# Performance work log

Hardware: AMD Instinct MI355X
Metric: run time of the kernel (lower is better)

## Reference

```python
import jax, jax.numpy as jnp
import numpy as np

K_LAYERS = 10
ALPHA = 0.1
N_NODES = 100_000
N_EDGES = 1_600_000
D_FEAT = 64


def setup_inputs() -> dict:
    key = jax.random.key(0)
    k1, k2, k3 = jax.random.split(key, 3)
    features = jax.random.normal(k1, (N_NODES, D_FEAT), dtype=jnp.float32)
    src = jax.random.randint(k2, (N_EDGES,), 0, N_NODES, dtype=jnp.int64)
    dst = jax.random.randint(k3, (N_EDGES,), 0, N_NODES, dtype=jnp.int64)
    return {"features": features, "src": src, "dst": dst}


def reference(features, src, dst):
    # APPNP forward (eval mode: feature dropout and edge_drop are identity).
    n = features.shape[0]
    ones = jnp.ones((src.shape[0],), dtype=features.dtype)
    deg_out = jax.ops.segment_sum(ones, src, num_segments=n)
    deg_in = jax.ops.segment_sum(ones, dst, num_segments=n)
    norm_src = jnp.clip(deg_out, 1.0) ** -0.5  # [N]
    norm_dst = jnp.clip(deg_in, 1.0) ** -0.5   # [N]

    h0 = features
    h = features
    for _ in range(K_LAYERS):
        # D_out^{-1/2} scaling, gather to edges, scatter-sum to dst, D_in^{-1/2}
        msg = (h * norm_src[:, None])[src]               # [E, d]
        agg = jax.ops.segment_sum(msg, dst, num_segments=n)  # [N, d]
        h = (1.0 - ALPHA) * (agg * norm_dst[:, None]) + ALPHA * h0
    return h
```

## Files before the change

kernel.cpp:

```cpp
#include <hip/hip_runtime.h>
#include <hip/hip_fp16.h>
#include <stdint.h>

#define D_FEAT 64
#define K_LAYERS 10
#define SCAN_CHUNK 2048
#define BINS 32768

__global__ __launch_bounds__(256) void deg_rank_hist_kernel(
    const int* __restrict__ src, const int* __restrict__ dst,
    int* deg_in, int* __restrict__ rank,
    unsigned short* __restrict__ Hsrc, int E, int N, int histBlocks)
{
    __shared__ unsigned ls[BINS / 4];
    int b = blockIdx.x;
    if (b >= histBlocks) {
        int i = (b - histBlocks) * blockDim.x + threadIdx.x;
        int base = i * 4;
        if (base + 3 < E) {
            int4 d4 = *(const int4*)(dst + base);
            int4 r;
            r.x = atomicAdd(&deg_in[d4.x], 1);
            r.y = atomicAdd(&deg_in[d4.y], 1);
            r.z = atomicAdd(&deg_in[d4.z], 1);
            r.w = atomicAdd(&deg_in[d4.w], 1);
            *(int4*)(rank + base) = r;
        } else {
            for (int j = base; j < E; ++j)
                rank[j] = atomicAdd(&deg_in[dst[j]], 1);
        }
    } else {
        int stripe = (((E + histBlocks - 1) / histBlocks) + 3) & ~3;
        int begin = b * stripe;
        int endb  = min(E, begin + stripe);
        int npass = (N + BINS - 1) / BINS;
        for (int p = 0; p < npass; ++p) {
            for (int j = threadIdx.x; j < BINS / 4; j += 256) ls[j] = 0;
            __syncthreads();
            unsigned lo = (unsigned)p * BINS;
            for (int q = begin + (int)threadIdx.x * 4; q < endb; q += 256 * 4) {
                if (q + 3 < endb) {
                    int4 s4 = *(const int4*)(src + q);
                    unsigned k;
                    k = (unsigned)s4.x - lo; if (k < BINS) atomicAdd(&ls[k >> 2], 1u << (8 * (k & 3)));
                    k = (unsigned)s4.y - lo; if (k < BINS) atomicAdd(&ls[k >> 2], 1u << (8 * (k & 3)));
                    k = (unsigned)s4.z - lo; if (k < BINS) atomicAdd(&ls[k >> 2], 1u << (8 * (k & 3)));
                    k = (unsigned)s4.w - lo; if (k < BINS) atomicAdd(&ls[k >> 2], 1u << (8 * (k & 3)));
                } else {
                    for (int t = q; t < endb; ++t) {
                        unsigned k = (unsigned)src[t] - lo;
                        if (k < BINS) atomicAdd(&ls[k >> 2], 1u << (8 * (k & 3)));
                    }
                }
            }
            __syncthreads();
            int nv = min(BINS, N - (int)lo);
            unsigned* HS = (unsigned*)(Hsrc + (size_t)b * N + lo);
            for (int j = threadIdx.x; j < nv / 4; j += 256) {
                unsigned w = ls[j];
                HS[2 * j]     = (w & 0xffu) | ((w >> 8) & 0xffu) << 16;
                HS[2 * j + 1] = ((w >> 16) & 0xffu) | ((w >> 24) & 0xffu) << 16;
            }
            __syncthreads();
        }
    }
}

__global__ void norm_kernel(const unsigned short* __restrict__ Hsrc,
                            const int* __restrict__ deg_in,
                            float* __restrict__ ns, float* __restrict__ nd,
                            float* __restrict__ cvec, int N, int histBlocks)
{
    int t = blockIdx.x * blockDim.x + threadIdx.x;
    int v0 = t * 4;
    if (v0 >= N) return;
    unsigned so[4] = {0, 0, 0, 0};
#pragma unroll 8
    for (int b = 0; b < histBlocks; ++b) {
        ushort4 h = *(const ushort4*)(Hsrc + (size_t)b * N + v0);
        so[0] += h.x; so[1] += h.y; so[2] += h.z; so[3] += h.w;
    }
    int4 di = *(const int4*)(deg_in + v0);
    float4 a, bb, cv;
    a.x = rsqrtf(fmaxf((float)so[0], 1.0f));
    a.y = rsqrtf(fmaxf((float)so[1], 1.0f));
    a.z = rsqrtf(fmaxf((float)so[2], 1.0f));
    a.w = rsqrtf(fmaxf((float)so[3], 1.0f));
    bb.x = rsqrtf(fmaxf((float)di.x, 1.0f));
    bb.y = rsqrtf(fmaxf((float)di.y, 1.0f));
    bb.z = rsqrtf(fmaxf((float)di.z, 1.0f));
    bb.w = rsqrtf(fmaxf((float)di.w, 1.0f));
    cv.x = 0.9f * a.x * bb.x;
    cv.y = 0.9f * a.y * bb.y;
    cv.z = 0.9f * a.z * bb.z;
    cv.w = 0.9f * a.w * bb.w;
    *(float4*)(ns + v0)   = a;
    *(float4*)(nd + v0)   = bb;
    *(float4*)(cvec + v0) = cv;
}

__global__ void chunk_sum_kernel(const int* __restrict__ deg, int N, int* __restrict__ partials) {
    __shared__ int sdata[256];
    constexpr int PT = SCAN_CHUNK / 256;
    int base = blockIdx.x * SCAN_CHUNK;
    int t = threadIdx.x;
    int s = 0;
#pragma unroll
    for (int j = 0; j < PT; ++j) {
        int idx = base + t * PT + j;
        if (idx < N) s += deg[idx];
    }
    sdata[t] = s;
    __syncthreads();
    for (int off = 128; off > 0; off >>= 1) {
        if (t < off) sdata[t] += sdata[t + off];
        __syncthreads();
    }
    if (t == 0) partials[blockIdx.x] = sdata[0];
}

__global__ void scan_partials_kernel(int* partials, int nchunks, int* row_ptr, int N, int E) {
    if (threadIdx.x == 0 && blockIdx.x == 0) {
        int s = 0;
        for (int i = 0; i < nchunks; ++i) { int v = partials[i]; partials[i] = s; s += v; }
        row_ptr[N] = E;
    }
}

__global__ void chunk_scan_kernel(const int* __restrict__ deg, int N,
                                  const int* __restrict__ partials, int* __restrict__ row_ptr) {
    __shared__ int sdata[256];
    constexpr int PT = SCAN_CHUNK / 256;
    int base = blockIdx.x * SCAN_CHUNK;
    int t = threadIdx.x;
    int vals[PT];
    int s = 0;
#pragma unroll
    for (int j = 0; j < PT; ++j) {
        int idx = base + t * PT + j;
        int v = (idx < N) ? deg[idx] : 0;
        vals[j] = s;
        s += v;
    }
    sdata[t] = s;
    __syncthreads();
    for (int off = 1; off < 256; off <<= 1) {
        int v = (t >= off) ? sdata[t - off] : 0;
        __syncthreads();
        sdata[t] += v;
        __syncthreads();
    }
    int texcl = (t > 0) ? sdata[t - 1] : 0;
    int off0 = partials[blockIdx.x];
#pragma unroll
    for (int j = 0; j < PT; ++j) {
        int idx = base + t * PT + j;
        if (idx < N) row_ptr[idx] = off0 + texcl + vals[j];
    }
}

__global__ void fill_cvt_kernel(const int* __restrict__ src, const int* __restrict__ dst,
                                const int* __restrict__ rank, const int* __restrict__ row_ptr,
                                unsigned* __restrict__ edge_src, int E, int fillBlocks,
                                const float* __restrict__ features, const float* __restrict__ ns,
                                __half* __restrict__ g0, __half* __restrict__ f0g, int N) {
    int b = blockIdx.x;
    if (b < fillBlocks) {
        int i = b * blockDim.x + threadIdx.x;
        int base = i * 4;
        if (base + 3 < E) {
            int4 s4 = *(const int4*)(src + base);
            int4 d4 = *(const int4*)(dst + base);
            int4 r4 = *(const int4*)(rank + base);
            edge_src[row_ptr[d4.x] + r4.x] = (unsigned)s4.x;
            edge_src[row_ptr[d4.y] + r4.y] = (unsigned)s4.y;
            edge_src[row_ptr[d4.z] + r4.z] = (unsigned)s4.z;
            edge_src[row_ptr[d4.w] + r4.w] = (unsigned)s4.w;
        } else {
            for (int j = base; j < E; ++j)
                edge_src[row_ptr[dst[j]] + rank[j]] = (unsigned)src[j];
        }
    } else {
        int t = (b - fillBlocks) * blockDim.x + threadIdx.x;
        if (t < N * (D_FEAT / 8)) {
            int node = t >> 3;
            float s = ns[node];
            float4 a = *((const float4*)features + 2 * t);
            float4 c = *((const float4*)features + 2 * t + 1);
            __half2 og[4], of[4];
            og[0] = __float22half2_rn(make_float2(s * a.x, s * a.y));
            og[1] = __float22half2_rn(make_float2(s * a.z, s * a.w));
            og[2] = __float22half2_rn(make_float2(s * c.x, s * c.y));
            og[3] = __float22half2_rn(make_float2(s * c.z, s * c.w));
            float sf = 0.1f * s;
            of[0] = __float22half2_rn(make_float2(sf * a.x, sf * a.y));
            of[1] = __float22half2_rn(make_float2(sf * a.z, sf * a.w));
            of[2] = __float22half2_rn(make_float2(sf * c.x, sf * c.y));
            of[3] = __float22half2_rn(make_float2(sf * c.z, sf * c.w));
            *((float4*)g0 + t)  = *(const float4*)og;
            *((float4*)f0g + t) = *(const float4*)of;
        }
    }
}

template <bool LAST>
__global__ __launch_bounds__(256) void prop_kernel(
    const __half* __restrict__ g, const __half* __restrict__ f0g,
    const float* __restrict__ features,
    const unsigned* __restrict__ edge_src, const int* __restrict__ row_ptr,
    const float* __restrict__ cvec, const float* __restrict__ nd,
    void* __restrict__ out, int N)
{
    int tid  = blockIdx.x * blockDim.x + threadIdx.x;
    int wave = tid >> 6;
    int lane = threadIdx.x & 63;
    int grp  = lane >> 3;
    int fl   = lane & 7;
    int node = wave * 8 + grp;
    if (node >= N) return;

    int e   = row_ptr[node];
    int end = row_ptr[node + 1];

    float acc[8];
#pragma unroll
    for (int j = 0; j < 8; ++j) acc[j] = 0.f;

    for (; e + 2 <= end; e += 2) {
        unsigned s0 = edge_src[e];
        unsigned s1 = edge_src[e + 1];
        float4 v0 = *((const float4*)(g + ((size_t)s0 << 6)) + fl);
        float4 v1 = *((const float4*)(g + ((size_t)s1 << 6)) + fl);
        const __half2* p0 = (const __half2*)&v0;
        const __half2* p1 = (const __half2*)&v1;
#pragma unroll
        for (int k = 0; k < 4; ++k) {
            float2 f0 = __half22float2(p0[k]);
            float2 f1 = __half22float2(p1[k]);
            acc[2 * k]     += f0.x + f1.x;
            acc[2 * k + 1] += f0.y + f1.y;
        }
    }
    if (e < end) {
        unsigned s0 = edge_src[e];
        float4 v0 = *((const float4*)(g + ((size_t)s0 << 6)) + fl);
        const __half2* p0 = (const __half2*)&v0;
#pragma unroll
        for (int k = 0; k < 4; ++k) {
            float2 f0 = __half22float2(p0[k]);
            acc[2 * k]     += f0.x;
            acc[2 * k + 1] += f0.y;
        }
    }

    if (!LAST) {
        float cm = cvec[node];
        float4 braw = *((const float4*)(f0g + ((size_t)node << 6)) + fl);
        const __half2* bp = (const __half2*)&braw;
        __half2 o[4];
#pragma unroll
        for (int k = 0; k < 4; ++k) {
            float2 f = __half22float2(bp[k]);
            o[k] = __float22half2_rn(make_float2(fmaf(cm, acc[2 * k], f.x),
                                                 fmaf(cm, acc[2 * k + 1], f.y)));
        }
        *((float4*)((__half*)out + ((size_t)node << 6)) + fl) = *(const float4*)o;
    } else {
        float w = 0.9f * nd[node];
        const float4* fp = (const float4*)(features + ((size_t)node << 6));
        float4 b0 = fp[2 * fl];
        float4 b1 = fp[2 * fl + 1];
        float4 o0, o1;
        o0.x = fmaf(w, acc[0], 0.1f * b0.x);
        o0.y = fmaf(w, acc[1], 0.1f * b0.y);
        o0.z = fmaf(w, acc[2], 0.1f * b0.z);
        o0.w = fmaf(w, acc[3], 0.1f * b0.w);
        o1.x = fmaf(w, acc[4], 0.1f * b1.x);
        o1.y = fmaf(w, acc[5], 0.1f * b1.y);
        o1.z = fmaf(w, acc[6], 0.1f * b1.z);
        o1.w = fmaf(w, acc[7], 0.1f * b1.w);
        float4* op = (float4*)((float*)out + ((size_t)node << 6));
        op[2 * fl]     = o0;
        op[2 * fl + 1] = o1;
    }
}

extern "C" void kernel_launch(void* const* d_in, const int* in_sizes, int n_in,
                              void* d_out, int out_size, void* d_ws, size_t ws_size,
                              hipStream_t stream) {
    const float* features = (const float*)d_in[0];
    const int*   src      = (const int*)d_in[1];
    const int*   dst      = (const int*)d_in[2];
    const int E = in_sizes[1];
    const int N = in_sizes[0] / D_FEAT;

    char* ws = (char*)d_ws;
    size_t off = 0;
    auto alloc = [&](size_t bytes, size_t align) -> char* {
        off = (off + align - 1) & ~(align - 1);
        char* p = ws + off;
        off += bytes;
        return p;
    };
    int*            deg_in    = (int*)alloc(4 * (size_t)N, 4);
    int*            row_ptr   = (int*)alloc(4 * ((size_t)N + 1), 4);
    float*          ns        = (float*)alloc(4 * (size_t)N, 4);
    float*          nd        = (float*)alloc(4 * (size_t)N, 4);
    float*          cvec      = (float*)alloc(4 * (size_t)N, 4);
    int nchunks = (N + SCAN_CHUNK - 1) / SCAN_CHUNK;
    int*            spartials = (int*)alloc(4 * (size_t)nchunks, 4);
    int*            rank      = (int*)alloc(4 * (size_t)E, 16);
    unsigned*       edge_src  = (unsigned*)alloc(4 * (size_t)E, 16);
    __half*         f0g       = (__half*)alloc(2 * (size_t)N * D_FEAT, 16);
    __half*         gA        = (__half*)alloc(2 * (size_t)N * D_FEAT, 16);
    __half*         gB        = (__half*)alloc(2 * (size_t)N * D_FEAT, 16);
    size_t remain = (ws_size > off + 1024) ? (ws_size - off - 1024) : 0;
    int HBr = (int)(remain / (2 * (size_t)N));
    HBr = HBr > 256 ? 256 : HBr;
    HBr = (HBr / 64) * 64;
    if (HBr < 64) HBr = 64;
    unsigned short* Hsrc = (unsigned short*)alloc(2 * (size_t)HBr * N, 16);

    (void)hipMemsetAsync(deg_in, 0, 4 * (size_t)N, stream);

    int ethreads4 = (E + 3) / 4;
    int eblocks = (ethreads4 + 255) / 256;
    deg_rank_hist_kernel<<<HBr + eblocks, 256, 0, stream>>>(src, dst, deg_in, rank, Hsrc, E, N, HBr);
    norm_kernel<<<(N / 4 + 255) / 256, 256, 0, stream>>>(Hsrc, deg_in, ns, nd, cvec, N, HBr);
    chunk_sum_kernel<<<nchunks, 256, 0, stream>>>(deg_in, N, spartials);
    scan_partials_kernel<<<1, 64, 0, stream>>>(spartials, nchunks, row_ptr, N, E);
    chunk_scan_kernel<<<nchunks, 256, 0, stream>>>(deg_in, N, spartials, row_ptr);

    int cvtThreads = N * (D_FEAT / 8);
    int cvtBlocks = (cvtThreads + 255) / 256;
    fill_cvt_kernel<<<eblocks + cvtBlocks, 256, 0, stream>>>(
        src, dst, rank, row_ptr, edge_src, E, eblocks, features, ns, gA, f0g, N);

    int waves = (N + 7) / 8;
    int prop_blocks = (waves * 64 + 255) / 256;
    const __half* h_in = gA;
    for (int k = 0; k < K_LAYERS - 1; ++k) {
        __half* h_out = (k & 1) ? gA : gB;
        prop_kernel<false><<<prop_blocks, 256, 0, stream>>>(
            h_in, f0g, features, edge_src, row_ptr, cvec, nd, h_out, N);
        h_in = h_out;
    }
    prop_kernel<true><<<prop_blocks, 256, 0, stream>>>(
        h_in, f0g, features, edge_src, row_ptr, cvec, nd, d_out, N);
}
```

Before: 672.6 us.

## Fuse all propagation layers into one persistent cooperative kernel with grid sync

Replaces the ten separate propagation launches with a single cooperative persistent kernel. It loops over layers, uses grid-stride node assignment and calls grid.sync between layers, ping-ponging the two half-precision buffers. This removes per-layer launch overhead and tail effects. In exchange it adds grid-wide barrier cost, and the grid is sized from occupancy (capped at 2048 blocks, assuming 256 CUs), so it may run with fewer waves in flight than the original launch.

```diff
diff --git a/kernel.cpp b/kernel.cpp
--- a/kernel.cpp
+++ b/kernel.cpp
@@ -1,6 +1,9 @@
 #include <hip/hip_runtime.h>
 #include <hip/hip_fp16.h>
+#include <hip/hip_cooperative_groups.h>
 #include <stdint.h>
+
+namespace cg = cooperative_groups;
 
 #define D_FEAT 64
 #define K_LAYERS 10
@@ -203,85 +206,95 @@
     }
 }
 
-template <bool LAST>
-__global__ __launch_bounds__(256) void prop_kernel(
-    const __half* __restrict__ g, const __half* __restrict__ f0g,
-    const float* __restrict__ features,
+__global__ __launch_bounds__(256, 8) void prop_persist_kernel(
+    __half* __restrict__ gA, __half* __restrict__ gB,
+    const __half* __restrict__ f0g, const float* __restrict__ features,
     const unsigned* __restrict__ edge_src, const int* __restrict__ row_ptr,
     const float* __restrict__ cvec, const float* __restrict__ nd,
-    void* __restrict__ out, int N)
+    float* __restrict__ out, int N)
 {
-    int tid  = blockIdx.x * blockDim.x + threadIdx.x;
-    int wave = tid >> 6;
-    int lane = threadIdx.x & 63;
-    int grp  = lane >> 3;
-    int fl   = lane & 7;
-    int node = wave * 8 + grp;
-    if (node >= N) return;
-
-    int e   = row_ptr[node];
-    int end = row_ptr[node + 1];
-
-    float acc[8];
-#pragma unroll
-    for (int j = 0; j < 8; ++j) acc[j] = 0.f;
-
-    for (; e + 2 <= end; e += 2) {
-        unsigned s0 = edge_src[e];
-        unsigned s1 = edge_src[e + 1];
-        float4 v0 = *((const float4*)(g + ((size_t)s0 << 6)) + fl);
-        float4 v1 = *((const float4*)(g + ((size_t)s1 << 6)) + fl);
-        const __half2* p0 = (const __half2*)&v0;
-        const __half2* p1 = (const __half2*)&v1;
-#pragma unroll
-        for (int k = 0; k < 4; ++k) {
-            float2 f0 = __half22float2(p0[k]);
-            float2 f1 = __half22float2(p1[k]);
-            acc[2 * k]     += f0.x + f1.x;
-            acc[2 * k + 1] += f0.y + f1.y;
-        }
-    }
-    if (e < end) {
-        unsigned s0 = edge_src[e];
-        float4 v0 = *((const float4*)(g + ((size_t)s0 << 6)) + fl);
-        const __half2* p0 = (const __half2*)&v0;
-#pragma unroll
-        for (int k = 0; k < 4; ++k) {
-            float2 f0 = __half22float2(p0[k]);
-            acc[2 * k]     += f0.x;
-            acc[2 * k + 1] += f0.y;
-        }
-    }
-
-    if (!LAST) {
-        float cm = cvec[node];
-        float4 braw = *((const float4*)(f0g + ((size_t)node << 6)) + fl);
-        const __half2* bp = (const __half2*)&braw;
-        __half2 o[4];
-#pragma unroll
-        for (int k = 0; k < 4; ++k) {
-            float2 f = __half22float2(bp[k]);
-            o[k] = __float22half2_rn(make_float2(fmaf(cm, acc[2 * k], f.x),
-                                                 fmaf(cm, acc[2 * k + 1], f.y)));
-        }
-        *((float4*)((__half*)out + ((size_t)node << 6)) + fl) = *(const float4*)o;
-    } else {
-        float w = 0.9f * nd[node];
-        const float4* fp = (const float4*)(features + ((size_t)node << 6));
-        float4 b0 = fp[2 * fl];
-        float4 b1 = fp[2 * fl + 1];
-        float4 o0, o1;
-        o0.x = fmaf(w, acc[0], 0.1f * b0.x);
-        o0.y = fmaf(w, acc[1], 0.1f * b0.y);
-        o0.z = fmaf(w, acc[2], 0.1f * b0.z);
-        o0.w = fmaf(w, acc[3], 0.1f * b0.w);
-        o1.x = fmaf(w, acc[4], 0.1f * b1.x);
-        o1.y = fmaf(w, acc[5], 0.1f * b1.y);
-        o1.z = fmaf(w, acc[6], 0.1f * b1.z);
-        o1.w = fmaf(w, acc[7], 0.1f * b1.w);
-        float4* op = (float4*)((float*)out + ((size_t)node << 6));
-        op[2 * fl]     = o0;
-        op[2 * fl + 1] = o1;
+    cg::grid_group grid = cg::this_grid();
+    int tid0    = blockIdx.x * blockDim.x + threadIdx.x;
+    int ggid    = tid0 >> 3;
+    int fl      = threadIdx.x & 7;
+    int nGroups = (gridDim.x * blockDim.x) >> 3;
+
+    const __half* h_in = gA;
+    __half*       h_out = gB;
+
+    for (int k = 0; k < K_LAYERS; ++k) {
+        bool last = (k == K_LAYERS - 1);
+        for (int node = ggid; node < N; node += nGroups) {
+            int e   = row_ptr[node];
+            int end = row_ptr[node + 1];
+            float acc[8];
+#pragma unroll
+            for (int j = 0; j < 8; ++j) acc[j] = 0.f;
+
+            for (; e + 2 <= end; e += 2) {
+                unsigned s0 = edge_src[e];
+                unsigned s1 = edge_src[e + 1];
+                float4 v0 = *((const float4*)(h_in + ((size_t)s0 << 6)) + fl);
+                float4 v1 = *((const float4*)(h_in + ((size_t)s1 << 6)) + fl);
+                const __half2* p0 = (const __half2*)&v0;
+                const __half2* p1 = (const __half2*)&v1;
+#pragma unroll
+                for (int kk = 0; kk < 4; ++kk) {
+                    float2 f0 = __half22float2(p0[kk]);
+                    float2 f1 = __half22float2(p1[kk]);
+                    acc[2 * kk]     += f0.x + f1.x;
+                    acc[2 * kk + 1] += f0.y + f1.y;
+                }
+            }
+            if (e < end) {
+                unsigned s0 = edge_src[e];
+                float4 v0 = *((const float4*)(h_in + ((size_t)s0 << 6)) + fl);
+                const __half2* p0 = (const __half2*)&v0;
+#pragma unroll
+                for (int kk = 0; kk < 4; ++kk) {
+                    float2 f0 = __half22float2(p0[kk]);
+                    acc[2 * kk]     += f0.x;
+                    acc[2 * kk + 1] += f0.y;
+                }
+            }
+
+            if (!last) {
+                float cm = cvec[node];
+                float4 braw = *((const float4*)(f0g + ((size_t)node << 6)) + fl);
+                const __half2* bp = (const __half2*)&braw;
+                __half2 o[4];
+#pragma unroll
+                for (int kk = 0; kk < 4; ++kk) {
+                    float2 f = __half22float2(bp[kk]);
+                    o[kk] = __float22half2_rn(make_float2(fmaf(cm, acc[2 * kk], f.x),
+                                                          fmaf(cm, acc[2 * kk + 1], f.y)));
+                }
+                *((float4*)(h_out + ((size_t)node << 6)) + fl) = *(const float4*)o;
+            } else {
+                float w = 0.9f * nd[node];
+                const float4* fp = (const float4*)(features + ((size_t)node << 6));
+                float4 b0 = fp[2 * fl];
+                float4 b1 = fp[2 * fl + 1];
+                float4 o0, o1;
+                o0.x = fmaf(w, acc[0], 0.1f * b0.x);
+                o0.y = fmaf(w, acc[1], 0.1f * b0.y);
+                o0.z = fmaf(w, acc[2], 0.1f * b0.z);
+                o0.w = fmaf(w, acc[3], 0.1f * b0.w);
+                o1.x = fmaf(w, acc[4], 0.1f * b1.x);
+                o1.y = fmaf(w, acc[5], 0.1f * b1.y);
+                o1.z = fmaf(w, acc[6], 0.1f * b1.z);
+                o1.w = fmaf(w, acc[7], 0.1f * b1.w);
+                float4* op = (float4*)(out + ((size_t)node << 6));
+                op[2 * fl]     = o0;
+                op[2 * fl + 1] = o1;
+            }
+        }
+        if (!last) {
+            grid.sync();
+            const __half* t = h_in;
+            h_in = h_out;
+            h_out = (__half*)t;
+        }
     }
 }
 
@@ -336,15 +349,14 @@
     fill_cvt_kernel<<<eblocks + cvtBlocks, 256, 0, stream>>>(
         src, dst, rank, row_ptr, edge_src, E, eblocks, features, ns, gA, f0g, N);
 
-    int waves = (N + 7) / 8;
-    int prop_blocks = (waves * 64 + 255) / 256;
-    const __half* h_in = gA;
-    for (int k = 0; k < K_LAYERS - 1; ++k) {
-        __half* h_out = (k & 1) ? gA : gB;
-        prop_kernel<false><<<prop_blocks, 256, 0, stream>>>(
-            h_in, f0g, features, edge_src, row_ptr, cvec, nd, h_out, N);
-        h_in = h_out;
-    }
-    prop_kernel<true><<<prop_blocks, 256, 0, stream>>>(
-        h_in, f0g, features, edge_src, row_ptr, cvec, nd, d_out, N);
-}
+    int maxBpc = 0;
+    (void)hipOccupancyMaxActiveBlocksPerMultiprocessor(&maxBpc, (const void*)prop_persist_kernel, 256, 0);
+    if (maxBpc < 1) maxBpc = 1;
+    int grid = maxBpc * 256;
+    if (grid > 2048) grid = 2048;
+
+    float* outp = (float*)d_out;
+    void* args[] = { &gA, &gB, &f0g, &features, &edge_src, &row_ptr, &cvec, &nd, &outp, (void*)&N };
+    (void)hipLaunchCooperativeKernel((const void*)prop_persist_kernel,
+                                     dim3(grid), dim3(256), args, 0, stream);
+}
```

After: 2.158 ms. +220.9%, slower.
